# Optimization experiments

Hardware: AMD Instinct MI355X
Metric: run time of the kernel (lower is better)

The kernel has to match this reference:

```python
import jax, jax.numpy as jnp
import numpy as np

DIM, N_HEADS, N_EXPERTS, TOP_K = 1024, 16, 8, 2
D_FF = 4 * DIM
HEAD_DIM = DIM // N_HEADS
EPS = 1e-5


def layer_norm(x, g, b):
    m = x.mean(-1, keepdims=True)
    v = ((x - m) ** 2).mean(-1, keepdims=True)
    return (x - m) / jnp.sqrt(v + EPS) * g + b


def setup_inputs() -> dict:
    key = jax.random.key(0)
    ks = jax.random.split(key, 16)
    B, T = 8, 1024
    s = 0.02
    inp = {
        'x': jax.random.normal(ks[0], (B, T, DIM), jnp.float32),
        'attention_mask': jnp.ones((B, T), jnp.int32),
        'Wq': jax.random.normal(ks[1], (DIM, DIM), jnp.float32) * s,
        'bq': jnp.zeros((DIM,), jnp.float32),
        'Wk': jax.random.normal(ks[2], (DIM, DIM), jnp.float32) * s,
        'bk': jnp.zeros((DIM,), jnp.float32),
        'Wv': jax.random.normal(ks[3], (DIM, DIM), jnp.float32) * s,
        'bv': jnp.zeros((DIM,), jnp.float32),
        'Wo': jax.random.normal(ks[4], (DIM, DIM), jnp.float32) * s,
        'bo': jnp.zeros((DIM,), jnp.float32),
        'g1': jnp.ones((DIM,), jnp.float32),
        'beta1': jnp.zeros((DIM,), jnp.float32),
        'router_w': jax.random.normal(ks[5], (DIM, N_EXPERTS), jnp.float32) * s,
        'router_b': jnp.zeros((N_EXPERTS,), jnp.float32),
        'W1': jax.random.normal(ks[6], (N_EXPERTS, DIM, D_FF), jnp.float32) * s,
        'B1': jnp.zeros((N_EXPERTS, D_FF), jnp.float32),
        'W2': jax.random.normal(ks[7], (N_EXPERTS, D_FF, DIM), jnp.float32) * s,
        'B2': jnp.zeros((N_EXPERTS, DIM), jnp.float32),
        'g2': jnp.ones((DIM,), jnp.float32),
        'beta2': jnp.zeros((DIM,), jnp.float32),
    }
    return inp


def reference(x, attention_mask, Wq, bq, Wk, bk, Wv, bv, Wo, bo, g1, beta1,
              router_w, router_b, W1, B1, W2, B2, g2, beta2):
    B, T, D = x.shape
    H, hd = N_HEADS, HEAD_DIM
    # ---- multi-head attention with causal + padding mask ----
    q = (x @ Wq + bq).reshape(B, T, H, hd).transpose(0, 2, 1, 3)  # [B,H,T,hd]
    k = (x @ Wk + bk).reshape(B, T, H, hd).transpose(0, 2, 1, 3)
    v = (x @ Wv + bv).reshape(B, T, H, hd).transpose(0, 2, 1, 3)
    scores = jnp.einsum('bhqd,bhkd->bhqk', q, k) / jnp.sqrt(jnp.float32(hd))
    causal = jnp.tril(jnp.ones((T, T), bool))[None, None]            # [1,1,T,T]
    mask = causal & (attention_mask[:, None, None, :] != 0)         # [B,1,T,T]
    scores = jnp.where(mask, scores, jnp.float32(-1e9))
    attn = jax.nn.softmax(scores, axis=-1)
    h = jnp.einsum('bhqk,bhkd->bhqd', attn, v).transpose(0, 2, 1, 3).reshape(B, T, D)
    h = h @ Wo + bo
    # dropout is identity in eval mode
    x1 = layer_norm(x + h, g1, beta1)
    # ---- sparse top-k MoE FFN ----
    xf = x1.reshape(-1, D)                                           # [N,D]
    logits = xf @ router_w + router_b                                # [N,E]
    probs = jax.nn.softmax(logits, axis=-1)
    topv, topi = jax.lax.top_k(probs, TOP_K)                         # [N,k]
    gk = topv / topv.sum(-1, keepdims=True)                          # renormalized gates
    onehot = jax.nn.one_hot(topi, N_EXPERTS, dtype=xf.dtype)         # [N,k,E]
    gates = (onehot * gk[..., None]).sum(1)                          # [N,E]
    y = jnp.zeros_like(xf)
    for e in range(N_EXPERTS):  # fixed small expert loop
        he = jax.nn.relu(xf @ W1[e] + B1[e])
        y = y + gates[:, e:e + 1] * (he @ W2[e] + B2[e])
    # load-balancing loss: E * sum_i f_i * P_i
    f = onehot.sum(1).mean(0)                                        # fraction routed per expert
    P = probs.mean(0)
    lb = jnp.float32(N_EXPERTS) * (f * P).sum()
    out = layer_norm(x1 + y.reshape(B, T, D), g2, beta2)
    return out, lb
```

## Files before the change

kernel.cpp:

```cpp
#include <hip/hip_runtime.h>
#include <hip/hip_bf16.h>
#include <stdint.h>

#define DIMQ   1024
#define NHEADS 16
#define HD     64
#define NEXP   8
#define DFF    4096
#define NTOK   8192
#define TSEQ   1024
#define BATCH  8

typedef unsigned short u16;
typedef unsigned int   u32;
typedef __attribute__((ext_vector_type(8))) short bf16x8;
typedef __attribute__((ext_vector_type(4))) float f32x4;

__device__ __forceinline__ float bf_lo(u32 w) { return __uint_as_float(w << 16); }
__device__ __forceinline__ float bf_hi(u32 w) { return __uint_as_float(w & 0xffff0000u); }
__device__ __forceinline__ u16 f2bf(float f) {
  u32 x = __float_as_uint(f);
  return (u16)((x + 0x7fffu + ((x >> 16) & 1u)) >> 16);
}

__device__ __forceinline__ void gload16(const u16* g, u16* l) {
  __builtin_amdgcn_global_load_lds((const __attribute__((address_space(1))) u32*)g,
                                   (__attribute__((address_space(3))) u32*)l, 16, 0, 0);
}

__global__ __launch_bounds__(256) void cvt_f32_bf16(const float* __restrict__ in,
                                                    u16* __restrict__ out, int n) {
  int i = (blockIdx.x * 256 + threadIdx.x) * 4;
  if (i >= n) return;
  float4 v = *(const float4*)(in + i);
  ushort4 o;
  o.x = f2bf(v.x); o.y = f2bf(v.y); o.z = f2bf(v.z); o.w = f2bf(v.w);
  *(ushort4*)(out + i) = o;
}

__global__ __launch_bounds__(256) void transpose_f32_bf16(
    const float* __restrict__ in, u16* __restrict__ out, int R, int C) {
  __shared__ float tile[32][33];
  size_t base = (size_t)blockIdx.z * (size_t)R * (size_t)C;
  int tx = threadIdx.x & 31, ty = threadIdx.x >> 5;
  int c = blockIdx.x * 32 + tx;
#pragma unroll
  for (int i = 0; i < 4; i++) {
    int r = blockIdx.y * 32 + ty + i * 8;
    tile[ty + i * 8][tx] = in[base + (size_t)r * C + c];
  }
  __syncthreads();
  int rr = blockIdx.y * 32 + tx;
#pragma unroll
  for (int i = 0; i < 4; i++) {
    int cc = blockIdx.x * 32 + ty + i * 8;
    out[base + (size_t)cc * R + rr] = f2bf(tile[tx][ty + i * 8]);
  }
}

template <bool GATHER, bool RELU, bool TRANSC>
__device__ __forceinline__ void gemm_core(
    const u16* __restrict__ A, const u16* __restrict__ Bt,
    const float* __restrict__ bias, u16* __restrict__ C,
    int M, int N, int K, const int* __restrict__ gidx) {
  __shared__ u16 As[3][128 * 32];
  __shared__ u16 Bs[3][128 * 32];
  const int tid = threadIdx.x;
  const int lane = tid & 63;
  const int wave = tid >> 6;
  const int wr = wave >> 1, wc = wave & 1;
  const int lr = lane & 15, kg = lane >> 4;
  const int rowbase = blockIdx.y * 128;
  const int colbase = blockIdx.x * 128;

  f32x4 acc[4][4];
#pragma unroll
  for (int m = 0; m < 4; m++)
#pragma unroll
    for (int n = 0; n < 4; n++) acc[m][n] = (f32x4){0.f, 0.f, 0.f, 0.f};

  const int r0 = tid >> 2, seg = tid & 3;
  const int slog = seg ^ ((r0 >> 1) & 3);
  int ar0 = rowbase + r0;      if (ar0 >= M) ar0 = M - 1;
  int ar1 = rowbase + r0 + 64; if (ar1 >= M) ar1 = M - 1;
  const long arow0 = GATHER ? gidx[ar0] : ar0;
  const long arow1 = GATHER ? gidx[ar1] : ar1;
  const u16* Aptr0 = A + (size_t)arow0 * K + slog * 8;
  const u16* Aptr1 = A + (size_t)arow1 * K + slog * 8;
  const u16* Bptr0 = Bt + (size_t)(colbase + r0) * K + slog * 8;
  const u16* Bptr1 = Bt + (size_t)(colbase + r0 + 64) * K + slog * 8;

  const int swz = (lr >> 1) & 3;

#define STAGE128(buf, k0)                                   \
  {                                                         \
    gload16(Aptr0 + (k0), &As[buf][tid * 8]);               \
    gload16(Aptr1 + (k0), &As[buf][2048 + tid * 8]);        \
    gload16(Bptr0 + (k0), &Bs[buf][tid * 8]);               \
    gload16(Bptr1 + (k0), &Bs[buf][2048 + tid * 8]);        \
  }

  const int NT = K >> 5;
  STAGE128(0, 0);
  STAGE128(1, 32);
  int cur = 0, stg = 2;
  for (int t = 0; t < NT; t++) {
    __syncthreads();
    if (t + 2 < NT) STAGE128(stg, (t + 2) << 5);
    bf16x8 af[4], bfr[4];
#pragma unroll
    for (int m = 0; m < 4; m++)
      af[m] = *(const bf16x8*)(&As[cur][(wr * 64 + m * 16 + lr) * 32 + ((kg ^ swz) * 8)]);
#pragma unroll
    for (int n = 0; n < 4; n++)
      bfr[n] = *(const bf16x8*)(&Bs[cur][(wc * 64 + n * 16 + lr) * 32 + ((kg ^ swz) * 8)]);
#pragma unroll
    for (int m = 0; m < 4; m++)
#pragma unroll
      for (int n = 0; n < 4; n++)
        acc[m][n] = __builtin_amdgcn_mfma_f32_16x16x32_bf16(af[m], bfr[n], acc[m][n], 0, 0, 0);
    cur = (cur == 2) ? 0 : cur + 1;
    stg = (stg == 2) ? 0 : stg + 1;
  }
#undef STAGE128

#pragma unroll
  for (int n = 0; n < 4; n++) {
    int col = colbase + wc * 64 + n * 16 + lr;
    float bv = bias[col];
#pragma unroll
    for (int m = 0; m < 4; m++) {
      int row0 = rowbase + wr * 64 + m * 16 + kg * 4;
      if (TRANSC) {
        if (row0 + 3 < M) {
          ushort4 pk;
          pk.x = f2bf(acc[m][n][0] + bv);
          pk.y = f2bf(acc[m][n][1] + bv);
          pk.z = f2bf(acc[m][n][2] + bv);
          pk.w = f2bf(acc[m][n][3] + bv);
          *(ushort4*)(&C[(size_t)col * M + row0]) = pk;
        } else {
#pragma unroll
          for (int r = 0; r < 4; r++)
            if (row0 + r < M) C[(size_t)col * M + row0 + r] = f2bf(acc[m][n][r] + bv);
        }
      } else {
#pragma unroll
        for (int r = 0; r < 4; r++) {
          int row = row0 + r;
          if (row < M) {
            float v = acc[m][n][r] + bv;
            if (RELU) v = fmaxf(v, 0.f);
            C[(size_t)row * N + col] = f2bf(v);
          }
        }
      }
    }
  }
}

__global__ __launch_bounds__(256) void gemm_bt_kernel(
    const u16* __restrict__ A, const u16* __restrict__ Bt,
    const float* __restrict__ bias, u16* __restrict__ C, int M, int N, int K) {
  gemm_core<false, false, false>(A, Bt, bias, C, M, N, K, nullptr);
}

__global__ __launch_bounds__(256) void gemm_bt_tc_kernel(
    const u16* __restrict__ A, const u16* __restrict__ Bt,
    const float* __restrict__ bias, u16* __restrict__ C, int M, int N, int K) {
  gemm_core<false, false, true>(A, Bt, bias, C, M, N, K, nullptr);
}

template <bool GATHER, bool RELU>
__device__ __forceinline__ void gemm256_core(
    const u16* __restrict__ A, const u16* __restrict__ Bt,
    const float* __restrict__ bias, u16* __restrict__ C,
    int M, int N, int K, const int* __restrict__ gidx) {
  __shared__ u16 As[3][256 * 32];
  __shared__ u16 Bs[3][256 * 32];
  const int tid = threadIdx.x;
  const int lane = tid & 63;
  const int wave = tid >> 6;
  const int wr = wave >> 2;
  const int wcol = wave & 3;
  const int lr = lane & 15, kg = lane >> 4;
  const int rowbase = blockIdx.y * 256;
  const int colbase = blockIdx.x * 256;

  f32x4 acc[8][4];
#pragma unroll
  for (int m = 0; m < 8; m++)
#pragma unroll
    for (int n = 0; n < 4; n++) acc[m][n] = (f32x4){0.f, 0.f, 0.f, 0.f};

  const u16* asrc[2];
  const u16* bsrc[2];
#pragma unroll
  for (int j = 0; j < 2; j++) {
    int p = tid + j * 512;
    int row = p >> 2, sphys = p & 3;
    int ls = sphys ^ ((row >> 1) & 3);
    int ar = rowbase + row; if (ar >= M) ar = M - 1;
    long ga = GATHER ? gidx[ar] : ar;
    asrc[j] = A + (size_t)ga * K + ls * 8;
    bsrc[j] = Bt + (size_t)(colbase + row) * K + ls * 8;
  }

#define STAGE256(buf, k0)                                      \
  {                                                            \
    gload16(asrc[0] + (k0), &As[buf][tid * 8]);                \
    gload16(asrc[1] + (k0), &As[buf][4096 + tid * 8]);         \
    gload16(bsrc[0] + (k0), &Bs[buf][tid * 8]);                \
    gload16(bsrc[1] + (k0), &Bs[buf][4096 + tid * 8]);         \
  }

  const int NT = K >> 5;
  STAGE256(0, 0);
  STAGE256(1, 32);
  int cur = 0, stg = 2;
  for (int t = 0; t < NT; t++) {
    __syncthreads();
    if (t + 2 < NT) STAGE256(stg, (t + 2) << 5);
    bf16x8 bfr[4];
#pragma unroll
    for (int nr = 0; nr < 4; nr++) {
      int rb = wcol * 64 + nr * 16 + lr;
      bfr[nr] = *(const bf16x8*)(&Bs[cur][rb * 32 + ((kg ^ ((rb >> 1) & 3)) * 8)]);
    }
#pragma unroll
    for (int mr = 0; mr < 8; mr++) {
      int ra = wr * 128 + mr * 16 + lr;
      bf16x8 a0 = *(const bf16x8*)(&As[cur][ra * 32 + ((kg ^ ((ra >> 1) & 3)) * 8)]);
#pragma unroll
      for (int nr = 0; nr < 4; nr++)
        acc[mr][nr] = __builtin_amdgcn_mfma_f32_16x16x32_bf16(a0, bfr[nr], acc[mr][nr], 0, 0, 0);
    }
    cur = (cur == 2) ? 0 : cur + 1;
    stg = (stg == 2) ? 0 : stg + 1;
  }
#undef STAGE256

#pragma unroll
  for (int nr = 0; nr < 4; nr++) {
    int col = colbase + wcol * 64 + nr * 16 + lr;
    float bv = bias[col];
#pragma unroll
    for (int mr = 0; mr < 8; mr++) {
      int row0 = rowbase + wr * 128 + mr * 16 + kg * 4;
#pragma unroll
      for (int r = 0; r < 4; r++) {
        int row = row0 + r;
        if (row < M) {
          float v = acc[mr][nr][r] + bv;
          if (RELU) v = fmaxf(v, 0.f);
          C[(size_t)row * N + col] = f2bf(v);
        }
      }
    }
  }
}

__global__ __launch_bounds__(512, 2) void moe_gemm1_kernel(
    const u16* __restrict__ x1b, const u16* __restrict__ W1t,
    const float* __restrict__ B1, u16* __restrict__ he,
    const int* __restrict__ cnt, const int* __restrict__ off,
    const int* __restrict__ idxlist) {
  int e = blockIdx.z;
  int M = cnt[e];
  if ((int)blockIdx.y * 256 >= M) return;
  gemm256_core<true, true>(x1b, W1t + (size_t)e * DFF * DIMQ, B1 + e * DFF,
                           he + (size_t)off[e] * DFF, M, DFF, DIMQ, idxlist + off[e]);
}

__global__ __launch_bounds__(512, 2) void moe_gemm2_kernel(
    const u16* __restrict__ he, const u16* __restrict__ W2t,
    const float* __restrict__ B2, u16* __restrict__ yslot,
    const int* __restrict__ cnt, const int* __restrict__ off) {
  int e = blockIdx.z;
  int M = cnt[e];
  if ((int)blockIdx.y * 256 >= M) return;
  gemm256_core<false, false>(he + (size_t)off[e] * DFF, W2t + (size_t)e * DIMQ * DFF,
                             B2 + e * DIMQ, yslot + (size_t)off[e] * DIMQ, M, DIMQ, DFF, nullptr);
}

__global__ __launch_bounds__(256) void attn_mfma_kernel(
    const u16* __restrict__ qb, const u16* __restrict__ kb,
    const u16* __restrict__ vbT, const int* __restrict__ amask,
    u16* __restrict__ hb) {
  __shared__ u16 Ks[64 * 64];
  __shared__ u16 VTs[64 * 64];
  __shared__ u16 Ps[4][16 * 64];
  __shared__ float mbias[64];

  const int b = blockIdx.y >> 4;
  const int h = blockIdx.y & 15;
  const int qb0 = blockIdx.x * 64;
  const int tid = threadIdx.x;
  const int lane = tid & 63;
  const int wq = tid >> 6;
  const int r16 = lane & 15;
  const int kg = lane >> 4;
  const int qrow0 = qb0 + wq * 16;

  bf16x8 qf[2];
  {
    const u16* qp = qb + ((size_t)(b * TSEQ + qrow0 + r16)) * DIMQ + h * HD + kg * 8;
    qf[0] = *(const bf16x8*)(qp);
    qf[1] = *(const bf16x8*)(qp + 32);
  }
  f32x4 acc[4];
#pragma unroll
  for (int db = 0; db < 4; db++) acc[db] = (f32x4){0.f, 0.f, 0.f, 0.f};
  float m_run[4], l_run[4];
#pragma unroll
  for (int i = 0; i < 4; i++) { m_run[i] = -3.0e38f; l_run[i] = 0.f; }

  const int kr0 = tid >> 3, ks0 = tid & 7;
  const int kr1 = (tid + 256) >> 3, ks1 = tid & 7;
  const u16* kgb = kb + (size_t)(b * TSEQ) * DIMQ + h * HD;
  const u16* vgb = vbT + (size_t)(h * HD) * NTOK + (size_t)b * TSEQ;

  const int nt = (qb0 + 64) >> 6;
  for (int kt = 0; kt < nt; kt++) {
    const int k0g = kt * 64;
    __syncthreads();
    {
      uint4 kv0 = *(const uint4*)(kgb + (size_t)(k0g + kr0) * DIMQ + ks0 * 8);
      *(uint4*)(&Ks[kr0 * 64 + ((ks0 ^ (kr0 & 7)) * 8)]) = kv0;
      uint4 kv1 = *(const uint4*)(kgb + (size_t)(k0g + kr1) * DIMQ + ks1 * 8);
      *(uint4*)(&Ks[kr1 * 64 + ((ks1 ^ (kr1 & 7)) * 8)]) = kv1;
      uint4 vv0 = *(const uint4*)(vgb + (size_t)kr0 * NTOK + k0g + ks0 * 8);
      *(uint4*)(&VTs[kr0 * 64 + ((ks0 ^ (kr0 & 7)) * 8)]) = vv0;
      uint4 vv1 = *(const uint4*)(vgb + (size_t)kr1 * NTOK + k0g + ks1 * 8);
      *(uint4*)(&VTs[kr1 * 64 + ((ks1 ^ (kr1 & 7)) * 8)]) = vv1;
      if (tid < 64) mbias[tid] = amask[b * TSEQ + k0g + tid] ? 0.f : -1e9f;
    }
    __syncthreads();
    if (k0g < qrow0 + 16) {
      f32x4 s[4];
#pragma unroll
      for (int g = 0; g < 4; g++) s[g] = (f32x4){0.f, 0.f, 0.f, 0.f};
#pragma unroll
      for (int g = 0; g < 4; g++) {
        int key = g * 16 + r16;
        bf16x8 ka  = *(const bf16x8*)(&Ks[key * 64 + ((kg ^ (key & 7)) * 8)]);
        bf16x8 kb2 = *(const bf16x8*)(&Ks[key * 64 + (((4 + kg) ^ (key & 7)) * 8)]);
        s[g] = __builtin_amdgcn_mfma_f32_16x16x32_bf16(qf[0], ka, s[g], 0, 0, 0);
        s[g] = __builtin_amdgcn_mfma_f32_16x16x32_bf16(qf[1], kb2, s[g], 0, 0, 0);
      }
      float mb[4] = {mbias[r16], mbias[16 + r16], mbias[32 + r16], mbias[48 + r16]};
      float sv[4][4], tm[4];
#pragma unroll
      for (int i = 0; i < 4; i++) {
        int qg = qrow0 + kg * 4 + i;
        tm[i] = -3.0e38f;
#pragma unroll
        for (int g = 0; g < 4; g++) {
          float a = s[g][i] * 0.125f + mb[g];
          if (k0g + g * 16 + r16 > qg) a = -3.0e38f;
          sv[g][i] = a;
          tm[i] = fmaxf(tm[i], a);
        }
      }
#pragma unroll
      for (int mk = 1; mk < 16; mk <<= 1) {
#pragma unroll
        for (int i = 0; i < 4; i++) tm[i] = fmaxf(tm[i], __shfl_xor(tm[i], mk));
      }
#pragma unroll
      for (int i = 0; i < 4; i++) {
        float nm = fmaxf(m_run[i], tm[i]);
        float sc = __expf(m_run[i] - nm);
        m_run[i] = nm;
        int qrl = kg * 4 + i;
        float lsum = 0.f;
#pragma unroll
        for (int g = 0; g < 4; g++) {
          float p = __expf(sv[g][i] - nm);
          lsum += p;
          int slotL = g * 2 + (r16 >> 3);
          Ps[wq][qrl * 64 + ((slotL ^ (qrl & 7)) * 8) + (r16 & 7)] = f2bf(p);
        }
        l_run[i] = l_run[i] * sc + lsum;
#pragma unroll
        for (int db = 0; db < 4; db++) acc[db][i] *= sc;
      }
      bf16x8 pf0 = *(const bf16x8*)(&Ps[wq][r16 * 64 + ((kg ^ (r16 & 7)) * 8)]);
      bf16x8 pf1 = *(const bf16x8*)(&Ps[wq][r16 * 64 + (((4 + kg) ^ (r16 & 7)) * 8)]);
#pragma unroll
      for (int db = 0; db < 4; db++) {
        int d = db * 16 + r16;
        bf16x8 vf0 = *(const bf16x8*)(&VTs[d * 64 + ((kg ^ (d & 7)) * 8)]);
        bf16x8 vf1 = *(const bf16x8*)(&VTs[d * 64 + (((4 + kg) ^ (d & 7)) * 8)]);
        acc[db] = __builtin_amdgcn_mfma_f32_16x16x32_bf16(pf0, vf0, acc[db], 0, 0, 0);
        acc[db] = __builtin_amdgcn_mfma_f32_16x16x32_bf16(pf1, vf1, acc[db], 0, 0, 0);
      }
    }
  }
#pragma unroll
  for (int mk = 1; mk < 16; mk <<= 1) {
#pragma unroll
    for (int i = 0; i < 4; i++) l_run[i] += __shfl_xor(l_run[i], mk);
  }
#pragma unroll
  for (int i = 0; i < 4; i++) {
    float inv = 1.f / l_run[i];
    int qg = qrow0 + kg * 4 + i;
    u16* op = hb + ((size_t)(b * TSEQ + qg)) * DIMQ + h * HD + r16;
#pragma unroll
    for (int db = 0; db < 4; db++) op[db * 16] = f2bf(acc[db][i] * inv);
  }
}

__global__ __launch_bounds__(256) void addln_kernel(
    const float* __restrict__ xin, const u16* __restrict__ hres,
    const float* __restrict__ g, const float* __restrict__ beta,
    float* __restrict__ x1, u16* __restrict__ x1b) {
  __shared__ float red[8];
  int t = blockIdx.x;
  int d = threadIdx.x * 4;
  size_t base = (size_t)t * DIMQ + d;
  float4 xv = *(const float4*)(xin + base);
  uint2 hu = *(const uint2*)(hres + base);
  float v0 = xv.x + bf_lo(hu.x), v1 = xv.y + bf_hi(hu.x);
  float v2 = xv.z + bf_lo(hu.y), v3 = xv.w + bf_hi(hu.y);
  float s1 = v0 + v1 + v2 + v3;
  float s2 = v0 * v0 + v1 * v1 + v2 * v2 + v3 * v3;
#pragma unroll
  for (int off = 32; off; off >>= 1) {
    s1 += __shfl_down(s1, off);
    s2 += __shfl_down(s2, off);
  }
  int w = threadIdx.x >> 6;
  if ((threadIdx.x & 63) == 0) { red[w] = s1; red[4 + w] = s2; }
  __syncthreads();
  float S1 = red[0] + red[1] + red[2] + red[3];
  float S2 = red[4] + red[5] + red[6] + red[7];
  float m = S1 * (1.f / DIMQ);
  float var = S2 * (1.f / DIMQ) - m * m;
  float rs = rsqrtf(var + 1e-5f);
  float4 gv = *(const float4*)(g + d);
  float4 bv = *(const float4*)(beta + d);
  float o0 = (v0 - m) * rs * gv.x + bv.x;
  float o1 = (v1 - m) * rs * gv.y + bv.y;
  float o2 = (v2 - m) * rs * gv.z + bv.z;
  float o3 = (v3 - m) * rs * gv.w + bv.w;
  *(float4*)(x1 + base) = make_float4(o0, o1, o2, o3);
  uint2 pu;
  pu.x = (u32)f2bf(o0) | ((u32)f2bf(o1) << 16);
  pu.y = (u32)f2bf(o2) | ((u32)f2bf(o3) << 16);
  *(uint2*)(x1b + base) = pu;
}

__global__ __launch_bounds__(256) void router_kernel(
    const float* __restrict__ x1, const float* __restrict__ rw,
    const float* __restrict__ rb, int* __restrict__ topi,
    float* __restrict__ gkout, float* __restrict__ probs) {
  int t = blockIdx.x * 4 + (threadIdx.x >> 6);
  int l = threadIdx.x & 63;
  float acc[8];
#pragma unroll
  for (int e = 0; e < 8; e++) acc[e] = 0.f;
  const float* xr = x1 + (size_t)t * DIMQ;
  for (int k = l; k < DIMQ; k += 64) {
    float xv = xr[k];
    const float* w = rw + (size_t)k * 8;
#pragma unroll
    for (int e = 0; e < 8; e++) acc[e] += xv * w[e];
  }
#pragma unroll
  for (int e = 0; e < 8; e++) {
#pragma unroll
    for (int off = 32; off; off >>= 1) acc[e] += __shfl_down(acc[e], off);
  }
  if (l == 0) {
    float lg[8], p[8];
    float mx = -3e38f;
#pragma unroll
    for (int e = 0; e < 8; e++) { lg[e] = acc[e] + rb[e]; mx = fmaxf(mx, lg[e]); }
    float sum = 0.f;
#pragma unroll
    for (int e = 0; e < 8; e++) { p[e] = expf(lg[e] - mx); sum += p[e]; }
    float isum = 1.f / sum;
#pragma unroll
    for (int e = 0; e < 8; e++) p[e] *= isum;
    int e0 = 0;
#pragma unroll
    for (int e = 1; e < 8; e++) if (p[e] > p[e0]) e0 = e;
    int e1 = (e0 == 0) ? 1 : 0;
#pragma unroll
    for (int e = 0; e < 8; e++) if (e != e0 && p[e] > p[e1]) e1 = e;
    float s2 = p[e0] + p[e1];
    topi[2 * t] = e0; topi[2 * t + 1] = e1;
    gkout[2 * t] = p[e0] / s2; gkout[2 * t + 1] = p[e1] / s2;
    float* pp = probs + (size_t)t * 8;
#pragma unroll
    for (int e = 0; e < 8; e++) pp[e] = p[e];
  }
}

__global__ __launch_bounds__(256) void stats_kernel(
    const float* __restrict__ probs, const int* __restrict__ topi,
    int* __restrict__ cnt, float* __restrict__ Psum) {
  __shared__ float sps[4][8];
  __shared__ int   slc[4][8];
  float ps[8];
  int lc[8];
#pragma unroll
  for (int e = 0; e < 8; e++) { ps[e] = 0.f; lc[e] = 0; }
  int t = blockIdx.x * 256 + threadIdx.x;
  {
    const float* p = probs + (size_t)t * 8;
#pragma unroll
    for (int e = 0; e < 8; e++) ps[e] += p[e];
    lc[topi[2 * t]]++;
    lc[topi[2 * t + 1]]++;
  }
#pragma unroll
  for (int e = 0; e < 8; e++) {
#pragma unroll
    for (int off = 32; off; off >>= 1) {
      ps[e] += __shfl_down(ps[e], off);
      lc[e] += __shfl_down(lc[e], off);
    }
  }
  int w = threadIdx.x >> 6;
  if ((threadIdx.x & 63) == 0) {
#pragma unroll
    for (int e = 0; e < 8; e++) { sps[w][e] = ps[e]; slc[w][e] = lc[e]; }
  }
  __syncthreads();
  if (threadIdx.x < 8) {
    float fp = sps[0][threadIdx.x] + sps[1][threadIdx.x] + sps[2][threadIdx.x] + sps[3][threadIdx.x];
    int   fc = slc[0][threadIdx.x] + slc[1][threadIdx.x] + slc[2][threadIdx.x] + slc[3][threadIdx.x];
    atomicAdd(&Psum[threadIdx.x], fp);
    atomicAdd(&cnt[threadIdx.x], fc);
  }
}

__global__ void offsets_kernel(const int* __restrict__ cnt, const float* __restrict__ Psum,
                               int* __restrict__ off, int* __restrict__ fill,
                               float* __restrict__ lb_out) {
  if (threadIdx.x == 0 && blockIdx.x == 0) {
    int o = 0;
    float lb = 0.f;
    for (int e = 0; e < NEXP; e++) {
      off[e] = o;
      fill[e] = o;
      o += cnt[e];
      lb += ((float)cnt[e] / (float)NTOK) * (Psum[e] / (float)NTOK);
    }
    lb_out[0] = (float)NEXP * lb;
  }
}

__global__ __launch_bounds__(256) void listbuild_kernel(
    const int* __restrict__ topi, int* fill, int* __restrict__ idxlist,
    int* __restrict__ posmap) {
  __shared__ int bcnt[8];
  __shared__ int base[8];
  __shared__ int bofs[8];
  int t = blockIdx.x * 256 + threadIdx.x;
  if (threadIdx.x < 8) { bcnt[threadIdx.x] = 0; bofs[threadIdx.x] = 0; }
  __syncthreads();
  int e0 = topi[2 * t], e1 = topi[2 * t + 1];
  atomicAdd(&bcnt[e0], 1);
  atomicAdd(&bcnt[e1], 1);
  __syncthreads();
  if (threadIdx.x < 8) base[threadIdx.x] = atomicAdd(&fill[threadIdx.x], bcnt[threadIdx.x]);
  __syncthreads();
  int s0 = base[e0] + atomicAdd(&bofs[e0], 1);
  idxlist[s0] = t;
  posmap[2 * t] = s0;
  int s1 = base[e1] + atomicAdd(&bofs[e1], 1);
  idxlist[s1] = t;
  posmap[2 * t + 1] = s1;
}

__global__ __launch_bounds__(256) void finalln_kernel(
    const float* __restrict__ x1, const u16* __restrict__ yslot,
    const int* __restrict__ posmap, const float* __restrict__ gkv,
    const float* __restrict__ g, const float* __restrict__ beta,
    float* __restrict__ out) {
  __shared__ float red[8];
  int t = blockIdx.x;
  int p0 = posmap[2 * t], p1 = posmap[2 * t + 1];
  float g0 = gkv[2 * t], g1 = gkv[2 * t + 1];
  int d = threadIdx.x * 4;
  size_t base = (size_t)t * DIMQ + d;
  float4 xv = *(const float4*)(x1 + base);
  uint2 y0 = *(const uint2*)(yslot + (size_t)p0 * DIMQ + d);
  uint2 y1 = *(const uint2*)(yslot + (size_t)p1 * DIMQ + d);
  float v0 = xv.x + g0 * bf_lo(y0.x) + g1 * bf_lo(y1.x);
  float v1 = xv.y + g0 * bf_hi(y0.x) + g1 * bf_hi(y1.x);
  float v2 = xv.z + g0 * bf_lo(y0.y) + g1 * bf_lo(y1.y);
  float v3 = xv.w + g0 * bf_hi(y0.y) + g1 * bf_hi(y1.y);
  float s1 = v0 + v1 + v2 + v3;
  float s2 = v0 * v0 + v1 * v1 + v2 * v2 + v3 * v3;
#pragma unroll
  for (int off = 32; off; off >>= 1) {
    s1 += __shfl_down(s1, off);
    s2 += __shfl_down(s2, off);
  }
  int w = threadIdx.x >> 6;
  if ((threadIdx.x & 63) == 0) { red[w] = s1; red[4 + w] = s2; }
  __syncthreads();
  float S1 = red[0] + red[1] + red[2] + red[3];
  float S2 = red[4] + red[5] + red[6] + red[7];
  float m = S1 * (1.f / DIMQ);
  float var = S2 * (1.f / DIMQ) - m * m;
  float rs = rsqrtf(var + 1e-5f);
  float4 gv = *(const float4*)(g + d);
  float4 bv = *(const float4*)(beta + d);
  float4 o;
  o.x = (v0 - m) * rs * gv.x + bv.x;
  o.y = (v1 - m) * rs * gv.y + bv.y;
  o.z = (v2 - m) * rs * gv.z + bv.z;
  o.w = (v3 - m) * rs * gv.w + bv.w;
  *(float4*)(out + base) = o;
}

extern "C" void kernel_launch(void* const* d_in, const int* in_sizes, int n_in,
                              void* d_out, int out_size, void* d_ws, size_t ws_size,
                              hipStream_t stream) {
  const float* x     = (const float*)d_in[0];
  const int*   amask = (const int*)d_in[1];
  const float* Wq    = (const float*)d_in[2];
  const float* bq    = (const float*)d_in[3];
  const float* Wk    = (const float*)d_in[4];
  const float* bk    = (const float*)d_in[5];
  const float* Wv    = (const float*)d_in[6];
  const float* bv    = (const float*)d_in[7];
  const float* Wo    = (const float*)d_in[8];
  const float* bo    = (const float*)d_in[9];
  const float* g1    = (const float*)d_in[10];
  const float* beta1 = (const float*)d_in[11];
  const float* rw    = (const float*)d_in[12];
  const float* rb    = (const float*)d_in[13];
  const float* W1    = (const float*)d_in[14];
  const float* B1    = (const float*)d_in[15];
  const float* W2    = (const float*)d_in[16];
  const float* B2    = (const float*)d_in[17];
  const float* g2    = (const float*)d_in[18];
  const float* beta2 = (const float*)d_in[19];
  float* out    = (float*)d_out;
  float* lb_out = out + (size_t)NTOK * DIMQ;

  char* ws = (char*)d_ws;
  size_t off_acc = 0;
  auto alloc = [&](size_t bytes) {
    void* p = ws + off_acc;
    off_acc += (bytes + 255) & ~(size_t)255;
    return p;
  };
  u16* xb    = (u16*)alloc((size_t)NTOK * DIMQ * 2);
  u16* qbuf  = (u16*)alloc((size_t)NTOK * DIMQ * 2);
  u16* kbuf  = (u16*)alloc((size_t)NTOK * DIMQ * 2);
  u16* vbufT = (u16*)alloc((size_t)NTOK * DIMQ * 2);
  u16* hb    = (u16*)alloc((size_t)NTOK * DIMQ * 2);
  u16* ho    = (u16*)alloc((size_t)NTOK * DIMQ * 2);
  float* x1  = (float*)alloc((size_t)NTOK * DIMQ * 4);
  u16* x1b   = (u16*)alloc((size_t)NTOK * DIMQ * 2);
  u16* Wqt   = (u16*)alloc((size_t)DIMQ * DIMQ * 2);
  u16* Wkt   = (u16*)alloc((size_t)DIMQ * DIMQ * 2);
  u16* Wvt   = (u16*)alloc((size_t)DIMQ * DIMQ * 2);
  u16* Wot   = (u16*)alloc((size_t)DIMQ * DIMQ * 2);
  u16* W1t   = (u16*)alloc((size_t)NEXP * DFF * DIMQ * 2);
  u16* W2t   = (u16*)alloc((size_t)NEXP * DIMQ * DFF * 2);
  u16* he    = (u16*)alloc((size_t)2 * NTOK * DFF * 2);
  u16* yslot = (u16*)alloc((size_t)2 * NTOK * DIMQ * 2);
  char* stats = (char*)alloc(4096);
  int*   cnt   = (int*)stats;
  float* Psum  = (float*)(stats + 32);
  int*   offp  = (int*)(stats + 64);
  int*   fill  = (int*)(stats + 96);
  int* topi    = (int*)alloc((size_t)NTOK * 2 * 4);
  float* gkbuf = (float*)alloc((size_t)NTOK * 2 * 4);
  int* posmap  = (int*)alloc((size_t)NTOK * 2 * 4);
  int* idxlist = (int*)alloc((size_t)NTOK * 2 * 4);
  float* probs = (float*)alloc((size_t)NTOK * 8 * 4);

  hipMemsetAsync(stats, 0, 64, stream);

  cvt_f32_bf16<<<NTOK * DIMQ / 1024, 256, 0, stream>>>(x, xb, NTOK * DIMQ);
  transpose_f32_bf16<<<dim3(DIMQ / 32, DIMQ / 32, 1), 256, 0, stream>>>(Wq, Wqt, DIMQ, DIMQ);
  transpose_f32_bf16<<<dim3(DIMQ / 32, DIMQ / 32, 1), 256, 0, stream>>>(Wk, Wkt, DIMQ, DIMQ);
  transpose_f32_bf16<<<dim3(DIMQ / 32, DIMQ / 32, 1), 256, 0, stream>>>(Wv, Wvt, DIMQ, DIMQ);
  transpose_f32_bf16<<<dim3(DIMQ / 32, DIMQ / 32, 1), 256, 0, stream>>>(Wo, Wot, DIMQ, DIMQ);
  transpose_f32_bf16<<<dim3(DFF / 32, DIMQ / 32, NEXP), 256, 0, stream>>>(W1, W1t, DIMQ, DFF);
  transpose_f32_bf16<<<dim3(DIMQ / 32, DFF / 32, NEXP), 256, 0, stream>>>(W2, W2t, DFF, DIMQ);

  dim3 gproj(DIMQ / 128, NTOK / 128);
  gemm_bt_kernel<<<gproj, 256, 0, stream>>>(xb, Wqt, bq, qbuf, NTOK, DIMQ, DIMQ);
  gemm_bt_kernel<<<gproj, 256, 0, stream>>>(xb, Wkt, bk, kbuf, NTOK, DIMQ, DIMQ);
  gemm_bt_tc_kernel<<<gproj, 256, 0, stream>>>(xb, Wvt, bv, vbufT, NTOK, DIMQ, DIMQ);
  attn_mfma_kernel<<<dim3(TSEQ / 64, BATCH * NHEADS), 256, 0, stream>>>(qbuf, kbuf, vbufT, amask, hb);
  gemm_bt_kernel<<<gproj, 256, 0, stream>>>(hb, Wot, bo, ho, NTOK, DIMQ, DIMQ);
  addln_kernel<<<NTOK, 256, 0, stream>>>(x, ho, g1, beta1, x1, x1b);

  router_kernel<<<NTOK / 4, 256, 0, stream>>>(x1, rw, rb, topi, gkbuf, probs);
  stats_kernel<<<NTOK / 256, 256, 0, stream>>>(probs, topi, cnt, Psum);
  offsets_kernel<<<1, 64, 0, stream>>>(cnt, Psum, offp, fill, lb_out);
  listbuild_kernel<<<NTOK / 256, 256, 0, stream>>>(topi, fill, idxlist, posmap);
  moe_gemm1_kernel<<<dim3(DFF / 256, 32, NEXP), 512, 0, stream>>>(x1b, W1t, B1, he, cnt, offp, idxlist);
  moe_gemm2_kernel<<<dim3(DIMQ / 256, 32, NEXP), 512, 0, stream>>>(he, W2t, B2, yslot, cnt, offp);
  finalln_kernel<<<NTOK, 256, 0, stream>>>(x1, yslot, posmap, gkbuf, g2, beta2, out);
}
```

Measured before the change: 1.040 ms.

## Replace triple-buffered GEMM pipeline with single-buffer BK=64 loop; drop 256-tile MoE GEMM

The 128x128 GEMM core moves from a 3-stage, BK=32 async prefetch pipeline to a single shared buffer with BK=64, an 8-way XOR swizzle, and two syncs per K step. The 256x256 tile kernel used for the MoE expert GEMMs is removed, and those GEMMs now use the 128x128 core with 256-thread blocks and a larger grid. The intent is better load balance and occupancy across experts with uneven token counts, and fewer barriers per K. The cost is that global-load latency is no longer overlapped with MFMA work, and the MoE GEMMs get less operand reuse per tile.

```diff
diff --git a/kernel.cpp b/kernel.cpp
--- a/kernel.cpp
+++ b/kernel.cpp
@@ -63,8 +63,8 @@
     const u16* __restrict__ A, const u16* __restrict__ Bt,
     const float* __restrict__ bias, u16* __restrict__ C,
     int M, int N, int K, const int* __restrict__ gidx) {
-  __shared__ u16 As[3][128 * 32];
-  __shared__ u16 Bs[3][128 * 32];
+  __shared__ u16 As[128 * 64];
+  __shared__ u16 Bs[128 * 64];
   const int tid = threadIdx.x;
   const int lane = tid & 63;
   const int wave = tid >> 6;
@@ -79,50 +79,47 @@
 #pragma unroll
     for (int n = 0; n < 4; n++) acc[m][n] = (f32x4){0.f, 0.f, 0.f, 0.f};
 
-  const int r0 = tid >> 2, seg = tid & 3;
-  const int slog = seg ^ ((r0 >> 1) & 3);
-  int ar0 = rowbase + r0;      if (ar0 >= M) ar0 = M - 1;
-  int ar1 = rowbase + r0 + 64; if (ar1 >= M) ar1 = M - 1;
-  const long arow0 = GATHER ? gidx[ar0] : ar0;
-  const long arow1 = GATHER ? gidx[ar1] : ar1;
-  const u16* Aptr0 = A + (size_t)arow0 * K + slog * 8;
-  const u16* Aptr1 = A + (size_t)arow1 * K + slog * 8;
-  const u16* Bptr0 = Bt + (size_t)(colbase + r0) * K + slog * 8;
-  const u16* Bptr1 = Bt + (size_t)(colbase + r0 + 64) * K + slog * 8;
-
-  const int swz = (lr >> 1) & 3;
-
-#define STAGE128(buf, k0)                                   \
-  {                                                         \
-    gload16(Aptr0 + (k0), &As[buf][tid * 8]);               \
-    gload16(Aptr1 + (k0), &As[buf][2048 + tid * 8]);        \
-    gload16(Bptr0 + (k0), &Bs[buf][tid * 8]);               \
-    gload16(Bptr1 + (k0), &Bs[buf][2048 + tid * 8]);        \
-  }
-
-  const int NT = K >> 5;
-  STAGE128(0, 0);
-  STAGE128(1, 32);
-  int cur = 0, stg = 2;
-  for (int t = 0; t < NT; t++) {
+  const u16* asrc[4];
+  const u16* bsrc[4];
+#pragma unroll
+  for (int j = 0; j < 4; j++) {
+    int p = tid + j * 256;
+    int row = p >> 3;
+    int ls = (p & 7) ^ (row & 7);
+    int ar = rowbase + row; if (ar >= M) ar = M - 1;
+    long ga = GATHER ? gidx[ar] : ar;
+    asrc[j] = A + (size_t)ga * K + ls * 8;
+    bsrc[j] = Bt + (size_t)(colbase + row) * K + ls * 8;
+  }
+
+  for (int k0 = 0; k0 < K; k0 += 64) {
+#pragma unroll
+    for (int j = 0; j < 4; j++) {
+      gload16(asrc[j] + k0, &As[(tid + j * 256) * 8]);
+      gload16(bsrc[j] + k0, &Bs[(tid + j * 256) * 8]);
+    }
     __syncthreads();
-    if (t + 2 < NT) STAGE128(stg, (t + 2) << 5);
-    bf16x8 af[4], bfr[4];
-#pragma unroll
-    for (int m = 0; m < 4; m++)
-      af[m] = *(const bf16x8*)(&As[cur][(wr * 64 + m * 16 + lr) * 32 + ((kg ^ swz) * 8)]);
-#pragma unroll
-    for (int n = 0; n < 4; n++)
-      bfr[n] = *(const bf16x8*)(&Bs[cur][(wc * 64 + n * 16 + lr) * 32 + ((kg ^ swz) * 8)]);
-#pragma unroll
-    for (int m = 0; m < 4; m++)
-#pragma unroll
-      for (int n = 0; n < 4; n++)
-        acc[m][n] = __builtin_amdgcn_mfma_f32_16x16x32_bf16(af[m], bfr[n], acc[m][n], 0, 0, 0);
-    cur = (cur == 2) ? 0 : cur + 1;
-    stg = (stg == 2) ? 0 : stg + 1;
-  }
-#undef STAGE128
+#pragma unroll
+    for (int h = 0; h < 2; h++) {
+      bf16x8 af[4], bfr[4];
+#pragma unroll
+      for (int m = 0; m < 4; m++) {
+        int ra = wr * 64 + m * 16 + lr;
+        af[m] = *(const bf16x8*)(&As[ra * 64 + (((h * 4 + kg) ^ (ra & 7)) * 8)]);
+      }
+#pragma unroll
+      for (int n = 0; n < 4; n++) {
+        int rb = wc * 64 + n * 16 + lr;
+        bfr[n] = *(const bf16x8*)(&Bs[rb * 64 + (((h * 4 + kg) ^ (rb & 7)) * 8)]);
+      }
+#pragma unroll
+      for (int m = 0; m < 4; m++)
+#pragma unroll
+        for (int n = 0; n < 4; n++)
+          acc[m][n] = __builtin_amdgcn_mfma_f32_16x16x32_bf16(af[m], bfr[n], acc[m][n], 0, 0, 0);
+    }
+    __syncthreads();
+  }
 
 #pragma unroll
   for (int n = 0; n < 4; n++) {
@@ -171,116 +168,27 @@
   gemm_core<false, false, true>(A, Bt, bias, C, M, N, K, nullptr);
 }
 
-template <bool GATHER, bool RELU>
-__device__ __forceinline__ void gemm256_core(
-    const u16* __restrict__ A, const u16* __restrict__ Bt,
-    const float* __restrict__ bias, u16* __restrict__ C,
-    int M, int N, int K, const int* __restrict__ gidx) {
-  __shared__ u16 As[3][256 * 32];
-  __shared__ u16 Bs[3][256 * 32];
-  const int tid = threadIdx.x;
-  const int lane = tid & 63;
-  const int wave = tid >> 6;
-  const int wr = wave >> 2;
-  const int wcol = wave & 3;
-  const int lr = lane & 15, kg = lane >> 4;
-  const int rowbase = blockIdx.y * 256;
-  const int colbase = blockIdx.x * 256;
-
-  f32x4 acc[8][4];
-#pragma unroll
-  for (int m = 0; m < 8; m++)
-#pragma unroll
-    for (int n = 0; n < 4; n++) acc[m][n] = (f32x4){0.f, 0.f, 0.f, 0.f};
-
-  const u16* asrc[2];
-  const u16* bsrc[2];
-#pragma unroll
-  for (int j = 0; j < 2; j++) {
-    int p = tid + j * 512;
-    int row = p >> 2, sphys = p & 3;
-    int ls = sphys ^ ((row >> 1) & 3);
-    int ar = rowbase + row; if (ar >= M) ar = M - 1;
-    long ga = GATHER ? gidx[ar] : ar;
-    asrc[j] = A + (size_t)ga * K + ls * 8;
-    bsrc[j] = Bt + (size_t)(colbase + row) * K + ls * 8;
-  }
-
-#define STAGE256(buf, k0)                                      \
-  {                                                            \
-    gload16(asrc[0] + (k0), &As[buf][tid * 8]);                \
-    gload16(asrc[1] + (k0), &As[buf][4096 + tid * 8]);         \
-    gload16(bsrc[0] + (k0), &Bs[buf][tid * 8]);                \
-    gload16(bsrc[1] + (k0), &Bs[buf][4096 + tid * 8]);         \
-  }
-
-  const int NT = K >> 5;
-  STAGE256(0, 0);
-  STAGE256(1, 32);
-  int cur = 0, stg = 2;
-  for (int t = 0; t < NT; t++) {
-    __syncthreads();
-    if (t + 2 < NT) STAGE256(stg, (t + 2) << 5);
-    bf16x8 bfr[4];
-#pragma unroll
-    for (int nr = 0; nr < 4; nr++) {
-      int rb = wcol * 64 + nr * 16 + lr;
-      bfr[nr] = *(const bf16x8*)(&Bs[cur][rb * 32 + ((kg ^ ((rb >> 1) & 3)) * 8)]);
-    }
-#pragma unroll
-    for (int mr = 0; mr < 8; mr++) {
-      int ra = wr * 128 + mr * 16 + lr;
-      bf16x8 a0 = *(const bf16x8*)(&As[cur][ra * 32 + ((kg ^ ((ra >> 1) & 3)) * 8)]);
-#pragma unroll
-      for (int nr = 0; nr < 4; nr++)
-        acc[mr][nr] = __builtin_amdgcn_mfma_f32_16x16x32_bf16(a0, bfr[nr], acc[mr][nr], 0, 0, 0);
-    }
-    cur = (cur == 2) ? 0 : cur + 1;
-    stg = (stg == 2) ? 0 : stg + 1;
-  }
-#undef STAGE256
-
-#pragma unroll
-  for (int nr = 0; nr < 4; nr++) {
-    int col = colbase + wcol * 64 + nr * 16 + lr;
-    float bv = bias[col];
-#pragma unroll
-    for (int mr = 0; mr < 8; mr++) {
-      int row0 = rowbase + wr * 128 + mr * 16 + kg * 4;
-#pragma unroll
-      for (int r = 0; r < 4; r++) {
-        int row = row0 + r;
-        if (row < M) {
-          float v = acc[mr][nr][r] + bv;
-          if (RELU) v = fmaxf(v, 0.f);
-          C[(size_t)row * N + col] = f2bf(v);
-        }
-      }
-    }
-  }
-}
-
-__global__ __launch_bounds__(512, 2) void moe_gemm1_kernel(
+__global__ __launch_bounds__(256) void moe_gemm1_kernel(
     const u16* __restrict__ x1b, const u16* __restrict__ W1t,
     const float* __restrict__ B1, u16* __restrict__ he,
     const int* __restrict__ cnt, const int* __restrict__ off,
     const int* __restrict__ idxlist) {
   int e = blockIdx.z;
   int M = cnt[e];
-  if ((int)blockIdx.y * 256 >= M) return;
-  gemm256_core<true, true>(x1b, W1t + (size_t)e * DFF * DIMQ, B1 + e * DFF,
-                           he + (size_t)off[e] * DFF, M, DFF, DIMQ, idxlist + off[e]);
-}
-
-__global__ __launch_bounds__(512, 2) void moe_gemm2_kernel(
+  if ((int)blockIdx.y * 128 >= M) return;
+  gemm_core<true, true, false>(x1b, W1t + (size_t)e * DFF * DIMQ, B1 + e * DFF,
+                               he + (size_t)off[e] * DFF, M, DFF, DIMQ, idxlist + off[e]);
+}
+
+__global__ __launch_bounds__(256) void moe_gemm2_kernel(
     const u16* __restrict__ he, const u16* __restrict__ W2t,
     const float* __restrict__ B2, u16* __restrict__ yslot,
     const int* __restrict__ cnt, const int* __restrict__ off) {
   int e = blockIdx.z;
   int M = cnt[e];
-  if ((int)blockIdx.y * 256 >= M) return;
-  gemm256_core<false, false>(he + (size_t)off[e] * DFF, W2t + (size_t)e * DIMQ * DFF,
-                             B2 + e * DIMQ, yslot + (size_t)off[e] * DIMQ, M, DIMQ, DFF, nullptr);
+  if ((int)blockIdx.y * 128 >= M) return;
+  gemm_core<false, false, false>(he + (size_t)off[e] * DFF, W2t + (size_t)e * DIMQ * DFF,
+                                 B2 + e * DIMQ, yslot + (size_t)off[e] * DIMQ, M, DIMQ, DFF, nullptr);
 }
 
 __global__ __launch_bounds__(256) void attn_mfma_kernel(
@@ -702,7 +610,7 @@
   stats_kernel<<<NTOK / 256, 256, 0, stream>>>(probs, topi, cnt, Psum);
   offsets_kernel<<<1, 64, 0, stream>>>(cnt, Psum, offp, fill, lb_out);
   listbuild_kernel<<<NTOK / 256, 256, 0, stream>>>(topi, fill, idxlist, posmap);
-  moe_gemm1_kernel<<<dim3(DFF / 256, 32, NEXP), 512, 0, stream>>>(x1b, W1t, B1, he, cnt, offp, idxlist);
-  moe_gemm2_kernel<<<dim3(DIMQ / 256, 32, NEXP), 512, 0, stream>>>(he, W2t, B2, yslot, cnt, offp);
+  moe_gemm1_kernel<<<dim3(DFF / 128, NTOK / 128, NEXP), 256, 0, stream>>>(x1b, W1t, B1, he, cnt, offp, idxlist);
+  moe_gemm2_kernel<<<dim3(DIMQ / 128, NTOK / 128, NEXP), 256, 0, stream>>>(he, W2t, B2, yslot, cnt, offp);
   finalln_kernel<<<NTOK, 256, 0, stream>>>(x1, yslot, posmap, gkbuf, g2, beta2, out);
 }
```

Result: faster. 957.3 us (-8.0%).

## Use BK=64 double-buffered MoE GEMM tiles with XCD-aware block remapping

Applied to the files above, without the earlier changes.

The 256x256 MoE GEMM tile now stages K=64 per step with two LDS buffers instead of K=32 with three, using an 8-way XOR swizzle. This halves the number of barriers and k-iterations. The 128 GEMM also moves from triple to double buffering. Block indices of the MoE GEMMs are remapped so that neighbouring tiles land on the same XCD, which should improve L2 reuse. The tradeoffs are that the double-buffered loop has less prefetch depth, and the remap assumes the grid size divides by 8. The early-exit check on M also now uses the remapped row index.

```diff
diff --git a/kernel.cpp b/kernel.cpp
--- a/kernel.cpp
+++ b/kernel.cpp
@@ -62,16 +62,15 @@
 __device__ __forceinline__ void gemm_core(
     const u16* __restrict__ A, const u16* __restrict__ Bt,
     const float* __restrict__ bias, u16* __restrict__ C,
-    int M, int N, int K, const int* __restrict__ gidx) {
-  __shared__ u16 As[3][128 * 32];
-  __shared__ u16 Bs[3][128 * 32];
+    int M, int N, int K, const int* __restrict__ gidx,
+    int rowbase, int colbase) {
+  __shared__ u16 As[2][128 * 32];
+  __shared__ u16 Bs[2][128 * 32];
   const int tid = threadIdx.x;
   const int lane = tid & 63;
   const int wave = tid >> 6;
   const int wr = wave >> 1, wc = wave & 1;
   const int lr = lane & 15, kg = lane >> 4;
-  const int rowbase = blockIdx.y * 128;
-  const int colbase = blockIdx.x * 128;
 
   f32x4 acc[4][4];
 #pragma unroll
@@ -102,25 +101,23 @@
 
   const int NT = K >> 5;
   STAGE128(0, 0);
-  STAGE128(1, 32);
-  int cur = 0, stg = 2;
+  __syncthreads();
   for (int t = 0; t < NT; t++) {
-    __syncthreads();
-    if (t + 2 < NT) STAGE128(stg, (t + 2) << 5);
+    const int buf = t & 1;
+    if (t + 1 < NT) STAGE128(buf ^ 1, (t + 1) << 5);
     bf16x8 af[4], bfr[4];
 #pragma unroll
     for (int m = 0; m < 4; m++)
-      af[m] = *(const bf16x8*)(&As[cur][(wr * 64 + m * 16 + lr) * 32 + ((kg ^ swz) * 8)]);
+      af[m] = *(const bf16x8*)(&As[buf][(wr * 64 + m * 16 + lr) * 32 + ((kg ^ swz) * 8)]);
 #pragma unroll
     for (int n = 0; n < 4; n++)
-      bfr[n] = *(const bf16x8*)(&Bs[cur][(wc * 64 + n * 16 + lr) * 32 + ((kg ^ swz) * 8)]);
+      bfr[n] = *(const bf16x8*)(&Bs[buf][(wc * 64 + n * 16 + lr) * 32 + ((kg ^ swz) * 8)]);
 #pragma unroll
     for (int m = 0; m < 4; m++)
 #pragma unroll
       for (int n = 0; n < 4; n++)
         acc[m][n] = __builtin_amdgcn_mfma_f32_16x16x32_bf16(af[m], bfr[n], acc[m][n], 0, 0, 0);
-    cur = (cur == 2) ? 0 : cur + 1;
-    stg = (stg == 2) ? 0 : stg + 1;
+    __syncthreads();
   }
 #undef STAGE128
 
@@ -162,30 +159,30 @@
 __global__ __launch_bounds__(256) void gemm_bt_kernel(
     const u16* __restrict__ A, const u16* __restrict__ Bt,
     const float* __restrict__ bias, u16* __restrict__ C, int M, int N, int K) {
-  gemm_core<false, false, false>(A, Bt, bias, C, M, N, K, nullptr);
+  gemm_core<false, false, false>(A, Bt, bias, C, M, N, K, nullptr,
+                                 blockIdx.y * 128, blockIdx.x * 128);
 }
 
 __global__ __launch_bounds__(256) void gemm_bt_tc_kernel(
     const u16* __restrict__ A, const u16* __restrict__ Bt,
     const float* __restrict__ bias, u16* __restrict__ C, int M, int N, int K) {
-  gemm_core<false, false, true>(A, Bt, bias, C, M, N, K, nullptr);
+  gemm_core<false, false, true>(A, Bt, bias, C, M, N, K, nullptr,
+                                blockIdx.y * 128, blockIdx.x * 128);
 }
 
 template <bool GATHER, bool RELU>
 __device__ __forceinline__ void gemm256_core(
     const u16* __restrict__ A, const u16* __restrict__ Bt,
     const float* __restrict__ bias, u16* __restrict__ C,
-    int M, int N, int K, const int* __restrict__ gidx) {
-  __shared__ u16 As[3][256 * 32];
-  __shared__ u16 Bs[3][256 * 32];
+    int M, int N, int K, const int* __restrict__ gidx,
+    int rowbase, int colbase) {
+  __shared__ u16 lds[2][2][256 * 64];
   const int tid = threadIdx.x;
   const int lane = tid & 63;
   const int wave = tid >> 6;
   const int wr = wave >> 2;
   const int wcol = wave & 3;
   const int lr = lane & 15, kg = lane >> 4;
-  const int rowbase = blockIdx.y * 256;
-  const int colbase = blockIdx.x * 256;
 
   f32x4 acc[8][4];
 #pragma unroll
@@ -193,50 +190,54 @@
 #pragma unroll
     for (int n = 0; n < 4; n++) acc[m][n] = (f32x4){0.f, 0.f, 0.f, 0.f};
 
-  const u16* asrc[2];
-  const u16* bsrc[2];
-#pragma unroll
-  for (int j = 0; j < 2; j++) {
-    int p = tid + j * 512;
-    int row = p >> 2, sphys = p & 3;
-    int ls = sphys ^ ((row >> 1) & 3);
+  const int srow0 = tid >> 3, sphys = tid & 7;
+  const u16* asrc[4];
+  const u16* bsrc[4];
+#pragma unroll
+  for (int j = 0; j < 4; j++) {
+    int row = srow0 + j * 64;
+    int ls = sphys ^ (row & 7);
     int ar = rowbase + row; if (ar >= M) ar = M - 1;
     long ga = GATHER ? gidx[ar] : ar;
     asrc[j] = A + (size_t)ga * K + ls * 8;
     bsrc[j] = Bt + (size_t)(colbase + row) * K + ls * 8;
   }
 
-#define STAGE256(buf, k0)                                      \
-  {                                                            \
-    gload16(asrc[0] + (k0), &As[buf][tid * 8]);                \
-    gload16(asrc[1] + (k0), &As[buf][4096 + tid * 8]);         \
-    gload16(bsrc[0] + (k0), &Bs[buf][tid * 8]);                \
-    gload16(bsrc[1] + (k0), &Bs[buf][4096 + tid * 8]);         \
-  }
-
-  const int NT = K >> 5;
+#define STAGE256(buf, k0)                                              \
+  {                                                                    \
+    _Pragma("unroll")                                                  \
+    for (int j = 0; j < 4; j++) {                                      \
+      gload16(asrc[j] + (k0), &lds[buf][0][tid * 8 + j * 4096]);       \
+      gload16(bsrc[j] + (k0), &lds[buf][1][tid * 8 + j * 4096]);       \
+    }                                                                  \
+  }
+
   STAGE256(0, 0);
-  STAGE256(1, 32);
-  int cur = 0, stg = 2;
+  __syncthreads();
+  const int NT = K >> 6;
   for (int t = 0; t < NT; t++) {
-    __syncthreads();
-    if (t + 2 < NT) STAGE256(stg, (t + 2) << 5);
-    bf16x8 bfr[4];
+    const int buf = t & 1;
+    if (t + 1 < NT) STAGE256(buf ^ 1, (t + 1) << 6);
+    bf16x8 bfr[4][2];
 #pragma unroll
     for (int nr = 0; nr < 4; nr++) {
       int rb = wcol * 64 + nr * 16 + lr;
-      bfr[nr] = *(const bf16x8*)(&Bs[cur][rb * 32 + ((kg ^ ((rb >> 1) & 3)) * 8)]);
+#pragma unroll
+      for (int kk = 0; kk < 2; kk++)
+        bfr[nr][kk] = *(const bf16x8*)(&lds[buf][1][rb * 64 + (((kk * 4 + kg) ^ (rb & 7)) * 8)]);
     }
 #pragma unroll
     for (int mr = 0; mr < 8; mr++) {
       int ra = wr * 128 + mr * 16 + lr;
-      bf16x8 a0 = *(const bf16x8*)(&As[cur][ra * 32 + ((kg ^ ((ra >> 1) & 3)) * 8)]);
-#pragma unroll
-      for (int nr = 0; nr < 4; nr++)
-        acc[mr][nr] = __builtin_amdgcn_mfma_f32_16x16x32_bf16(a0, bfr[nr], acc[mr][nr], 0, 0, 0);
+      bf16x8 a0 = *(const bf16x8*)(&lds[buf][0][ra * 64 + ((kg ^ (ra & 7)) * 8)]);
+      bf16x8 a1 = *(const bf16x8*)(&lds[buf][0][ra * 64 + (((4 + kg) ^ (ra & 7)) * 8)]);
+#pragma unroll
+      for (int nr = 0; nr < 4; nr++) {
+        acc[mr][nr] = __builtin_amdgcn_mfma_f32_16x16x32_bf16(a0, bfr[nr][0], acc[mr][nr], 0, 0, 0);
+        acc[mr][nr] = __builtin_amdgcn_mfma_f32_16x16x32_bf16(a1, bfr[nr][1], acc[mr][nr], 0, 0, 0);
+      }
     }
-    cur = (cur == 2) ? 0 : cur + 1;
-    stg = (stg == 2) ? 0 : stg + 1;
+    __syncthreads();
   }
 #undef STAGE256
 
@@ -260,6 +261,15 @@
   }
 }
 
+__device__ __forceinline__ void xcd_remap(int& bx, int& by) {
+  int gx = gridDim.x, gy = gridDim.y;
+  int wg = by * gx + bx;
+  int cpx = (gx * gy) >> 3;
+  int sz = (wg & 7) * cpx + (wg >> 3);
+  bx = sz % gx;
+  by = sz / gx;
+}
+
 __global__ __launch_bounds__(512, 2) void moe_gemm1_kernel(
     const u16* __restrict__ x1b, const u16* __restrict__ W1t,
     const float* __restrict__ B1, u16* __restrict__ he,
@@ -267,9 +277,12 @@
     const int* __restrict__ idxlist) {
   int e = blockIdx.z;
   int M = cnt[e];
-  if ((int)blockIdx.y * 256 >= M) return;
+  int bx = blockIdx.x, by = blockIdx.y;
+  xcd_remap(bx, by);
+  if (by * 256 >= M) return;
   gemm256_core<true, true>(x1b, W1t + (size_t)e * DFF * DIMQ, B1 + e * DFF,
-                           he + (size_t)off[e] * DFF, M, DFF, DIMQ, idxlist + off[e]);
+                           he + (size_t)off[e] * DFF, M, DFF, DIMQ, idxlist + off[e],
+                           by * 256, bx * 256);
 }
 
 __global__ __launch_bounds__(512, 2) void moe_gemm2_kernel(
@@ -278,9 +291,12 @@
     const int* __restrict__ cnt, const int* __restrict__ off) {
   int e = blockIdx.z;
   int M = cnt[e];
-  if ((int)blockIdx.y * 256 >= M) return;
+  int bx = blockIdx.x, by = blockIdx.y;
+  xcd_remap(bx, by);
+  if (by * 256 >= M) return;
   gemm256_core<false, false>(he + (size_t)off[e] * DFF, W2t + (size_t)e * DIMQ * DFF,
-                             B2 + e * DIMQ, yslot + (size_t)off[e] * DIMQ, M, DIMQ, DFF, nullptr);
+                             B2 + e * DIMQ, yslot + (size_t)off[e] * DIMQ, M, DIMQ, DFF, nullptr,
+                             by * 256, bx * 256);
 }
 
 __global__ __launch_bounds__(256) void attn_mfma_kernel(
```

Result: slower. 1.535 ms (+47.6%).
